# Optimization experiments

Measured on AMD Instinct MI355X. Metric: run time of the kernel, lower is better.

## Reference

```python
import jax, jax.numpy as jnp
import numpy as np

N_NODES = 32768
N_EDGES = 524288
N_FEAT = 256
HID = 256
N_GRAPHS = 64
N_CLASSES = 4
NODES_PER_GRAPH = N_NODES // N_GRAPHS
BN_EPS = 1e-5


def setup_inputs() -> dict:
    key = jax.random.key(0)
    ks = jax.random.split(key, 16)
    x = jax.random.normal(ks[0], (N_NODES, N_FEAT), dtype=jnp.float32)
    edge_index = jax.random.randint(ks[1], (2, N_EDGES), 0, N_NODES, dtype=jnp.int32)
    batch = (jnp.arange(N_NODES, dtype=jnp.int32) // NODES_PER_GRAPH)
    def xavier(k, shape):
        fan_in, fan_out = shape[0], shape[1]
        a = float(np.sqrt(6.0 / (fan_in + fan_out)))
        return jax.random.uniform(k, shape, jnp.float32, -a, a)
    return {
        "x": x, "edge_index": edge_index, "batch": batch,
        "W1": xavier(ks[2], (N_FEAT, HID)), "b1": jnp.zeros((HID,), jnp.float32),
        "g1": jnp.ones((HID,), jnp.float32), "be1": jnp.zeros((HID,), jnp.float32),
        "W2": xavier(ks[3], (HID, HID)), "b2": jnp.zeros((HID,), jnp.float32),
        "g2": jnp.ones((HID,), jnp.float32), "be2": jnp.zeros((HID,), jnp.float32),
        "W_ih": xavier(ks[4], (HID, 4 * HID)), "W_hh": xavier(ks[5], (HID, 4 * HID)),
        "b_ih": jnp.zeros((4 * HID,), jnp.float32), "b_hh": jnp.zeros((4 * HID,), jnp.float32),
        "W_fc": xavier(ks[6], (HID, N_CLASSES)), "b_fc": jnp.zeros((N_CLASSES,), jnp.float32),
    }


def gcn_conv(x, W, b, src, dst):
    # PyG GCNConv: add self-loops, symmetric normalization, aggregate, then bias
    h = x @ W                                   # [N, H]
    deg = jnp.zeros((x.shape[0],), h.dtype).at[dst].add(1.0) + 1.0  # in-deg + self-loop
    dinv = jax.lax.rsqrt(deg)
    coef = dinv[src] * dinv[dst]                # [E]
    msg = h[src] * coef[:, None]                # gather + scale, [E, H]
    agg = jnp.zeros_like(h).at[dst].add(msg)    # scatter-add
    agg = agg + h * (1.0 / deg)[:, None]        # self-loop term (norm = 1/deg)
    return agg + b


def batch_norm(x, gamma, beta):
    mean = jnp.mean(x, axis=0)
    var = jnp.mean(jnp.square(x - mean), axis=0)  # biased, as torch BN training
    return (x - mean) * jax.lax.rsqrt(var + BN_EPS) * gamma + beta


def reference(x, edge_index, batch, W1, b1, g1, be1, W2, b2, g2, be2,
              W_ih, W_hh, b_ih, b_hh, W_fc, b_fc):
    src, dst = edge_index[0], edge_index[1]
    h = jax.nn.relu(batch_norm(gcn_conv(x, W1, b1, src, dst), g1, be1))
    h = jax.nn.relu(batch_norm(gcn_conv(h, W2, b2, src, dst), g2, be2))
    # global mean pool over graphs
    sums = jax.ops.segment_sum(h, batch, num_segments=N_GRAPHS)
    cnts = jax.ops.segment_sum(jnp.ones((h.shape[0],), h.dtype), batch, num_segments=N_GRAPHS)
    pooled = sums / cnts[:, None]               # [G, H]
    # LSTM, seq_len = 1, zero initial state -> single cell step
    h0 = jnp.zeros((N_GRAPHS, HID), h.dtype)
    c0 = jnp.zeros((N_GRAPHS, HID), h.dtype)
    gates = pooled @ W_ih + h0 @ W_hh + b_ih + b_hh  # [G, 4H]
    i, f, g, o = jnp.split(gates, 4, axis=1)
    c1 = jax.nn.sigmoid(f) * c0 + jax.nn.sigmoid(i) * jnp.tanh(g)
    h1 = jax.nn.sigmoid(o) * jnp.tanh(c1)
    logits = h1 @ W_fc + b_fc
    logp = jax.nn.log_softmax(logits, axis=1)
    return (logp, (h1[None], c1[None]))
```

## Files before the change

kernel.cpp:

```cpp
#include <hip/hip_runtime.h>
#include <math.h>

#define N_NODES 32768
#define N_FEAT 256
#define HID 256
#define N_GRAPHS 64
#define NPG 512
#define N_CLASSES 4
#define BN_EPS 1e-5f

typedef __attribute__((ext_vector_type(8))) short bf16x8;
typedef __attribute__((ext_vector_type(4))) float f32x4;

__device__ __forceinline__ ushort f2b(float f) {
    union { float f; uint u; } v; v.f = f;
    uint u = v.u;
    return (ushort)((u + 0x7FFFu + ((u >> 16) & 1u)) >> 16);
}
__device__ __forceinline__ float bflo(uint u) {
    union { uint u; float f; } v; v.u = u << 16;
    return v.f;
}
__device__ __forceinline__ float bfhi(uint u) {
    union { uint u; float f; } v; v.u = u & 0xFFFF0000u;
    return v.f;
}

__global__ void k_count_prep(const int* __restrict__ dst, int* __restrict__ degcnt, int cntB,
                             const float* __restrict__ x, ushort* __restrict__ xb, int xB,
                             const float* __restrict__ W1, const float* __restrict__ W2,
                             ushort* __restrict__ Wt1, ushort* __restrict__ Wt2,
                             uint* __restrict__ csrs, int E) {
    int b = blockIdx.x;
    int t = threadIdx.x;
    if (b < cntB) {
        int e = b * 256 + t;
        if (e < E) atomicAdd(&degcnt[dst[e]], 1);
    } else if (b < cntB + xB) {
        int i = (b - cntB) * 256 + t;
        float4 v0 = *(const float4*)(x + (size_t)i * 8);
        float4 v1 = *(const float4*)(x + (size_t)i * 8 + 4);
        uint4 o;
        o.x = (uint)f2b(v0.x) | ((uint)f2b(v0.y) << 16);
        o.y = (uint)f2b(v0.z) | ((uint)f2b(v0.w) << 16);
        o.z = (uint)f2b(v1.x) | ((uint)f2b(v1.y) << 16);
        o.w = (uint)f2b(v1.z) | ((uint)f2b(v1.w) << 16);
        *(uint4*)(xb + (size_t)i * 8) = o;
    } else if (b < cntB + xB + 512) {
        int wb = b - cntB - xB;
        const float* W = (wb < 256) ? W1 : W2;
        ushort* Wt = (wb < 256) ? Wt1 : Wt2;
        int n = wb & 255;
        Wt[n * 256 + t] = f2b(W[t * 256 + n]);
    } else {
        int i = (b - cntB - xB - 512) * 256 + t;
        uint4 s = make_uint4(N_NODES, N_NODES, N_NODES, N_NODES);
        *(uint4*)(csrs + (size_t)i * 4) = s;
    }
}

__global__ __launch_bounds__(1024) void k_scan_all(const int* __restrict__ degcnt,
                                                   float* __restrict__ dinv,
                                                   int* __restrict__ row_start,
                                                   int* __restrict__ cursor,
                                                   uint* __restrict__ csrs,
                                                   ushort* __restrict__ hs_pad) {
    __shared__ int wsum[16];
    int t = threadIdx.x;
    int base = t * 32;
    int s = 0;
#pragma unroll
    for (int i = 0; i < 32; ++i) {
        int c = degcnt[base + i];
        s += (c + 2) & ~1;
    }
    int lane = t & 63, w = t >> 6;
    int v = s;
    for (int off = 1; off < 64; off <<= 1) {
        int u = __shfl_up(v, off);
        if (lane >= off) v += u;
    }
    if (lane == 63) wsum[w] = v;
    __syncthreads();
    if (t < 16) {
        int x = wsum[t];
        for (int off = 1; off < 16; off <<= 1) {
            int u = __shfl_up(x, off, 16);
            if (t >= off) x += u;
        }
        wsum[t] = x;
    }
    __syncthreads();
    int run = ((w > 0) ? wsum[w - 1] : 0) + v - s;
    for (int i = 0; i < 32; ++i) {
        int n = base + i;
        int c = degcnt[n];
        row_start[n] = run;
        csrs[run] = (uint)n;
        cursor[n] = run + 1;
        dinv[n] = rsqrtf((float)(c + 1));
        run += (c + 2) & ~1;
    }
    if (t == 0) row_start[N_NODES] = wsum[15];
    if (t < 128) ((uint*)hs_pad)[t] = 0;
}

__global__ void k_fill(const int* __restrict__ src, const int* __restrict__ dst,
                       int* __restrict__ cursor, uint* __restrict__ csrs, int E) {
    int e = blockIdx.x * 256 + threadIdx.x;
    if (e >= E) return;
    int d = dst[e];
    int pos = atomicAdd(&cursor[d], 1);
    csrs[pos] = (uint)src[e];
}

__global__ __launch_bounds__(256) void k_gemm_bf16(const ushort* __restrict__ A,
                                                   const ushort* __restrict__ Bt,
                                                   const float* __restrict__ dinv,
                                                   ushort* __restrict__ hs) {
    __shared__ ushort Bs[128 * 256];
    int tid = threadIdx.x;
    int n0 = blockIdx.x * 128;
    int m0 = blockIdx.y * 128;

#pragma unroll
    for (int c = 0; c < 16; ++c) {
        int g = c * 256 + tid;
        int idx = g * 8;
        int row = idx >> 8;
        int col = idx & 255;
        uint4 v = *(const uint4*)(Bt + (size_t)(n0 + row) * 256 + col);
        int sidx = idx ^ ((row & 7) << 3);
        *(uint4*)(Bs + sidx) = v;
    }
    __syncthreads();

    int wid = tid >> 6;
    int lane = tid & 63;
    int wr = wid >> 1, wc = wid & 1;
    int r = lane & 15;
    int ko = (lane >> 4) * 8;

    const ushort* Ab = A + (size_t)(m0 + wr * 64 + r) * 256 + ko;

    f32x4 acc[4][4] = {};
#pragma unroll
    for (int ks = 0; ks < 8; ++ks) {
        bf16x8 a[4], b[4];
#pragma unroll
        for (int i = 0; i < 4; ++i)
            a[i] = *(const bf16x8*)(Ab + i * (16 * 256) + ks * 32);
#pragma unroll
        for (int j = 0; j < 4; ++j) {
            int srow = wc * 64 + j * 16 + r;
            int idx = (srow * 256 + ko + ks * 32) ^ ((srow & 7) << 3);
            b[j] = *(const bf16x8*)(Bs + idx);
        }
#pragma unroll
        for (int i = 0; i < 4; ++i)
#pragma unroll
            for (int j = 0; j < 4; ++j)
                acc[i][j] = __builtin_amdgcn_mfma_f32_16x16x32_bf16(a[i], b[j], acc[i][j], 0, 0, 0);
    }

    int rr = (lane >> 4) * 4;
    int cc = lane & 15;
#pragma unroll
    for (int i = 0; i < 4; ++i) {
        int row = m0 + wr * 64 + i * 16 + rr;
#pragma unroll
        for (int r2 = 0; r2 < 4; ++r2) {
            float dv = dinv[row + r2];
#pragma unroll
            for (int j = 0; j < 4; ++j) {
                int col = n0 + wc * 64 + j * 16 + cc;
                hs[(size_t)(row + r2) * 256 + col] = f2b(acc[i][j][r2] * dv);
            }
        }
    }
}

__global__ __launch_bounds__(256) void k_agg(const ushort* __restrict__ hs,
                                             const uint* __restrict__ csrs,
                                             const int* __restrict__ row_start,
                                             const float* __restrict__ dinv,
                                             const float* __restrict__ bias,
                                             ushort* __restrict__ aggb) {
    int wid = threadIdx.x >> 6;
    int lane = threadIdx.x & 63;
    int half = lane >> 5;
    int fq = lane & 31;
    int n = blockIdx.x * 4 + wid;

    float dv = dinv[n];
    int base = row_start[n];
    int pairs = (row_start[n + 1] - base) >> 1;

    float a0 = 0.f, a1 = 0.f, a2 = 0.f, a3 = 0.f, a4 = 0.f, a5 = 0.f, a6 = 0.f, a7 = 0.f;

    int t = 0;
    for (; t + 4 <= pairs; t += 4) {
        uint s0 = csrs[base + 2 * t + 0 + half];
        uint s1 = csrs[base + 2 * t + 2 + half];
        uint s2 = csrs[base + 2 * t + 4 + half];
        uint s3 = csrs[base + 2 * t + 6 + half];
        uint4 h0 = *(const uint4*)(hs + (size_t)s0 * 256 + fq * 8);
        uint4 h1 = *(const uint4*)(hs + (size_t)s1 * 256 + fq * 8);
        uint4 h2 = *(const uint4*)(hs + (size_t)s2 * 256 + fq * 8);
        uint4 h3 = *(const uint4*)(hs + (size_t)s3 * 256 + fq * 8);
        a0 += bflo(h0.x) + bflo(h1.x) + bflo(h2.x) + bflo(h3.x);
        a1 += bfhi(h0.x) + bfhi(h1.x) + bfhi(h2.x) + bfhi(h3.x);
        a2 += bflo(h0.y) + bflo(h1.y) + bflo(h2.y) + bflo(h3.y);
        a3 += bfhi(h0.y) + bfhi(h1.y) + bfhi(h2.y) + bfhi(h3.y);
        a4 += bflo(h0.z) + bflo(h1.z) + bflo(h2.z) + bflo(h3.z);
        a5 += bfhi(h0.z) + bfhi(h1.z) + bfhi(h2.z) + bfhi(h3.z);
        a6 += bflo(h0.w) + bflo(h1.w) + bflo(h2.w) + bflo(h3.w);
        a7 += bfhi(h0.w) + bfhi(h1.w) + bfhi(h2.w) + bfhi(h3.w);
    }
    for (; t < pairs; ++t) {
        uint s0 = csrs[base + 2 * t + half];
        uint4 h0 = *(const uint4*)(hs + (size_t)s0 * 256 + fq * 8);
        a0 += bflo(h0.x); a1 += bfhi(h0.x);
        a2 += bflo(h0.y); a3 += bfhi(h0.y);
        a4 += bflo(h0.z); a5 += bfhi(h0.z);
        a6 += bflo(h0.w); a7 += bfhi(h0.w);
    }

    a0 += __shfl_xor(a0, 32); a1 += __shfl_xor(a1, 32);
    a2 += __shfl_xor(a2, 32); a3 += __shfl_xor(a3, 32);
    a4 += __shfl_xor(a4, 32); a5 += __shfl_xor(a5, 32);
    a6 += __shfl_xor(a6, 32); a7 += __shfl_xor(a7, 32);

    if (half == 0) {
        float4 b0 = *(const float4*)&bias[fq * 8];
        float4 b1 = *(const float4*)&bias[fq * 8 + 4];
        float o0 = a0 * dv + b0.x, o1 = a1 * dv + b0.y;
        float o2 = a2 * dv + b0.z, o3 = a3 * dv + b0.w;
        float o4 = a4 * dv + b1.x, o5 = a5 * dv + b1.y;
        float o6 = a6 * dv + b1.z, o7 = a7 * dv + b1.w;
        uint4 ov;
        ov.x = (uint)f2b(o0) | ((uint)f2b(o1) << 16);
        ov.y = (uint)f2b(o2) | ((uint)f2b(o3) << 16);
        ov.z = (uint)f2b(o4) | ((uint)f2b(o5) << 16);
        ov.w = (uint)f2b(o6) | ((uint)f2b(o7) << 16);
        *(uint4*)(aggb + (size_t)n * HID + fq * 8) = ov;
    }
}

__global__ __launch_bounds__(256) void k_bn_stats(const ushort* __restrict__ aggb,
                                                  float* __restrict__ bnsum,
                                                  float* __restrict__ bnsq) {
    int t = threadIdx.x;
    int fq = t & 31;
    int rg = t >> 5;
    int r0 = blockIdx.x * 128 + rg * 16;

    float s[8] = {}, q[8] = {};
    for (int r = 0; r < 16; ++r) {
        uint4 v = *(const uint4*)(aggb + (size_t)(r0 + r) * HID + fq * 8);
        float f0 = bflo(v.x), f1 = bfhi(v.x), f2 = bflo(v.y), f3 = bfhi(v.y);
        float f4 = bflo(v.z), f5 = bfhi(v.z), f6 = bflo(v.w), f7 = bfhi(v.w);
        s[0] += f0; q[0] += f0 * f0;  s[1] += f1; q[1] += f1 * f1;
        s[2] += f2; q[2] += f2 * f2;  s[3] += f3; q[3] += f3 * f3;
        s[4] += f4; q[4] += f4 * f4;  s[5] += f5; q[5] += f5 * f5;
        s[6] += f6; q[6] += f6 * f6;  s[7] += f7; q[7] += f7 * f7;
    }

    __shared__ float red[8][32][16];
#pragma unroll
    for (int i = 0; i < 8; ++i) {
        red[rg][fq][i] = s[i];
        red[rg][fq][8 + i] = q[i];
    }
    __syncthreads();
    int fq2 = t & 31;
    int vg = t >> 5;
#pragma unroll
    for (int k = 0; k < 2; ++k) {
        int v = vg * 2 + k;
        float acc = 0.f;
#pragma unroll
        for (int rgi = 0; rgi < 8; ++rgi) acc += red[rgi][fq2][v];
        float* dstp = (v < 8) ? bnsum : bnsq;
        atomicAdd(&dstp[fq2 * 8 + (v & 7)], acc);
    }
}

__global__ void k_bn_apply_b(const ushort* __restrict__ x, const float* __restrict__ bnsum,
                             const float* __restrict__ bnsq, const float* __restrict__ gamma,
                             const float* __restrict__ beta, ushort* __restrict__ out) {
    int i = blockIdx.x * 256 + threadIdx.x;
    if (i >= N_NODES * HID / 4) return;
    int f = (i & 63) * 4;
    const float invN = 1.0f / (float)N_NODES;
    uint2 v = *(const uint2*)(x + (size_t)i * 4);
    float vv[4] = {bflo(v.x), bfhi(v.x), bflo(v.y), bfhi(v.y)};
    float r[4];
#pragma unroll
    for (int qq = 0; qq < 4; ++qq) {
        float mean = bnsum[f + qq] * invN;
        float var = bnsq[f + qq] * invN - mean * mean;
        float t = (vv[qq] - mean) * rsqrtf(var + BN_EPS) * gamma[f + qq] + beta[f + qq];
        r[qq] = t > 0.0f ? t : 0.0f;
    }
    uint2 o;
    o.x = (uint)f2b(r[0]) | ((uint)f2b(r[1]) << 16);
    o.y = (uint)f2b(r[2]) | ((uint)f2b(r[3]) << 16);
    *(uint2*)(out + (size_t)i * 4) = o;
}

__global__ __launch_bounds__(256) void k_bn_pool(const ushort* __restrict__ aggb,
                                                 const float* __restrict__ bnsum,
                                                 const float* __restrict__ bnsq,
                                                 const float* __restrict__ gamma,
                                                 const float* __restrict__ beta,
                                                 float* __restrict__ pooled) {
    int g = blockIdx.x >> 4;
    int blk = blockIdx.x & 15;
    int f = threadIdx.x;
    const float invN = 1.0f / (float)N_NODES;
    float mean = bnsum[f] * invN;
    float var = bnsq[f] * invN - mean * mean;
    float sc = rsqrtf(var + BN_EPS) * gamma[f];
    float sh = beta[f] - mean * sc;
    int r0 = g * NPG + blk * 32;
    float s = 0.0f;
#pragma unroll 4
    for (int r = 0; r < 32; ++r) {
        float v = bflo((uint)aggb[(size_t)(r0 + r) * HID + f]) * sc + sh;
        s += v > 0.0f ? v : 0.0f;
    }
    atomicAdd(&pooled[g * HID + f], s);
}

__global__ __launch_bounds__(256) void k_head(const float* __restrict__ pooled,
                                              const float* __restrict__ W_ih,
                                              const float* __restrict__ b_ih,
                                              const float* __restrict__ b_hh,
                                              const float* __restrict__ W_fc,
                                              const float* __restrict__ b_fc,
                                              float* __restrict__ out) {
    __shared__ float p[HID];
    __shared__ float lsum[N_CLASSES][256];
    __shared__ float logits[N_CLASSES];
    int g = blockIdx.x, j = threadIdx.x;
    p[j] = pooled[g * HID + j] * (1.0f / (float)NPG);
    __syncthreads();

    float gi = 0.f, gf = 0.f, gg = 0.f, go = 0.f;
#pragma unroll 4
    for (int k = 0; k < HID; ++k) {
        float pk = p[k];
        const float* w = &W_ih[(size_t)k * (4 * HID) + j];
        gi += pk * w[0];
        gf += pk * w[HID];
        gg += pk * w[2 * HID];
        go += pk * w[3 * HID];
    }
    gi += b_ih[j] + b_hh[j];
    gf += b_ih[HID + j] + b_hh[HID + j];
    gg += b_ih[2 * HID + j] + b_hh[2 * HID + j];
    go += b_ih[3 * HID + j] + b_hh[3 * HID + j];
    (void)gf;

    float si = 1.f / (1.f + expf(-gi));
    float so = 1.f / (1.f + expf(-go));
    float c1 = si * tanhf(gg);
    float h1 = so * tanhf(c1);

    out[N_GRAPHS * N_CLASSES + g * HID + j] = h1;
    out[N_GRAPHS * N_CLASSES + N_GRAPHS * HID + g * HID + j] = c1;

#pragma unroll
    for (int c = 0; c < N_CLASSES; ++c)
        lsum[c][j] = h1 * W_fc[j * N_CLASSES + c];
    __syncthreads();
    for (int s = 128; s > 0; s >>= 1) {
        if (j < s) {
#pragma unroll
            for (int c = 0; c < N_CLASSES; ++c)
                lsum[c][j] += lsum[c][j + s];
        }
        __syncthreads();
    }
    if (j < N_CLASSES) logits[j] = lsum[j][0] + b_fc[j];
    __syncthreads();
    if (j < N_CLASSES) {
        float m = fmaxf(fmaxf(logits[0], logits[1]), fmaxf(logits[2], logits[3]));
        float lse = m + logf(expf(logits[0] - m) + expf(logits[1] - m) +
                             expf(logits[2] - m) + expf(logits[3] - m));
        out[g * N_CLASSES + j] = logits[j] - lse;
    }
}

extern "C" void kernel_launch(void* const* d_in, const int* in_sizes, int n_in,
                              void* d_out, int out_size, void* d_ws, size_t ws_size,
                              hipStream_t stream) {
    const float* x    = (const float*)d_in[0];
    const int*   ei   = (const int*)d_in[1];
    const float* W1   = (const float*)d_in[3];
    const float* b1   = (const float*)d_in[4];
    const float* g1   = (const float*)d_in[5];
    const float* be1  = (const float*)d_in[6];
    const float* W2   = (const float*)d_in[7];
    const float* b2   = (const float*)d_in[8];
    const float* g2   = (const float*)d_in[9];
    const float* be2  = (const float*)d_in[10];
    const float* W_ih = (const float*)d_in[11];
    const float* b_ih = (const float*)d_in[13];
    const float* b_hh = (const float*)d_in[14];
    const float* W_fc = (const float*)d_in[15];
    const float* b_fc = (const float*)d_in[16];
    float* out = (float*)d_out;

    int E = in_sizes[1] / 2;
    const int* src = ei;
    const int* dst = ei + E;

    const size_t MAT = (size_t)N_NODES * HID;
    size_t SZ = ((size_t)E + 2 * N_NODES + 1023) & ~(size_t)1023;

    ushort* aggb = (ushort*)d_ws;
    ushort* xb   = aggb + MAT;
    ushort* hs   = xb + MAT;
    ushort* Wt1  = hs + MAT + 256;
    ushort* Wt2  = Wt1 + 65536;
    float*  dinv = (float*)(Wt2 + 65536);
    int*    row_start = (int*)(dinv + N_NODES);
    int*    cursor    = row_start + N_NODES + 2;
    uint*   csrs      = (uint*)(cursor + N_NODES);
    int*    degcnt = (int*)(csrs + SZ);
    float*  bn1sum = (float*)(degcnt + N_NODES);
    float*  bn1sq  = bn1sum + HID;
    float*  bn2sum = bn1sq + HID;
    float*  bn2sq  = bn2sum + HID;
    float*  pooled = bn2sq + HID;
    size_t zeroBytes = (size_t)N_NODES * 4 + 4 * HID * 4 + (size_t)N_GRAPHS * HID * 4;

    dim3 blk(256);
    int edgeBlocks = (E + 255) / 256;
    int n8blk = (int)(MAT / 8 / 256);
    int sentB = (int)(SZ / 1024);
    int vec4Blocks = (int)(MAT / 4 / 256);
    int aggBlocks = N_NODES / 4;
    dim3 gemmGrid(2, N_NODES / 128);

    hipMemsetAsync(degcnt, 0, zeroBytes, stream);

    k_count_prep<<<edgeBlocks + n8blk + 512 + sentB, blk, 0, stream>>>(
        dst, degcnt, edgeBlocks, x, xb, n8blk, W1, W2, Wt1, Wt2, csrs, E);
    k_scan_all<<<1, dim3(1024), 0, stream>>>(degcnt, dinv, row_start, cursor, csrs,
                                             hs + MAT);
    k_fill<<<edgeBlocks, blk, 0, stream>>>(src, dst, cursor, csrs, E);

    k_gemm_bf16<<<gemmGrid, blk, 0, stream>>>(xb, Wt1, dinv, hs);
    k_agg<<<aggBlocks, blk, 0, stream>>>(hs, csrs, row_start, dinv, b1, aggb);
    k_bn_stats<<<N_NODES / 128, blk, 0, stream>>>(aggb, bn1sum, bn1sq);
    k_bn_apply_b<<<vec4Blocks, blk, 0, stream>>>(aggb, bn1sum, bn1sq, g1, be1, xb);

    k_gemm_bf16<<<gemmGrid, blk, 0, stream>>>(xb, Wt2, dinv, hs);
    k_agg<<<aggBlocks, blk, 0, stream>>>(hs, csrs, row_start, dinv, b2, aggb);
    k_bn_stats<<<N_NODES / 128, blk, 0, stream>>>(aggb, bn2sum, bn2sq);
    k_bn_pool<<<N_GRAPHS * 16, blk, 0, stream>>>(aggb, bn2sum, bn2sq, g2, be2, pooled);

    k_head<<<N_GRAPHS, blk, 0, stream>>>(pooled, W_ih, b_ih, b_hh, W_fc, b_fc, out);
}
```

Before: 324.1 us.

## Replace single-block degree scan with three-pass multi-block prefix scan

The single 1024-thread block that scanned all 32768 degree counts and wrote row_start, cursor, csrs sentinels and dinv is split into three kernels: per-block reduction, a 128-entry block-offset scan, and a parallel per-node scan-and-write across 128 blocks. The old kernel ran serial 32-element loops per thread on one CU, with strided writes that coalesce poorly. The new path spreads that work over many CUs at the cost of two extra kernel launches and a round trip through global memory for the block sums.

```diff
diff --git a/kernel.cpp b/kernel.cpp
--- a/kernel.cpp
+++ b/kernel.cpp
@@ -59,50 +59,69 @@
     }
 }
 
-__global__ __launch_bounds__(1024) void k_scan_all(const int* __restrict__ degcnt,
-                                                   float* __restrict__ dinv,
-                                                   int* __restrict__ row_start,
-                                                   int* __restrict__ cursor,
-                                                   uint* __restrict__ csrs,
-                                                   ushort* __restrict__ hs_pad) {
-    __shared__ int wsum[16];
+__global__ __launch_bounds__(256) void k_scan1(const int* __restrict__ degcnt,
+                                               int* __restrict__ blocksum) {
+    int n = blockIdx.x * 256 + threadIdx.x;
+    int p = (degcnt[n] + 2) & ~1;
+#pragma unroll
+    for (int off = 1; off < 64; off <<= 1) p += __shfl_xor(p, off);
+    __shared__ int ws[4];
+    int lane = threadIdx.x & 63, w = threadIdx.x >> 6;
+    if (lane == 0) ws[w] = p;
+    __syncthreads();
+    if (threadIdx.x == 0)
+        blocksum[blockIdx.x] = ws[0] + ws[1] + ws[2] + ws[3];
+}
+
+__global__ __launch_bounds__(128) void k_scan2(const int* __restrict__ blocksum,
+                                               int* __restrict__ blockoff,
+                                               int* __restrict__ row_start,
+                                               ushort* __restrict__ hs_pad) {
     int t = threadIdx.x;
-    int base = t * 32;
-    int s = 0;
-#pragma unroll
-    for (int i = 0; i < 32; ++i) {
-        int c = degcnt[base + i];
-        s += (c + 2) & ~1;
-    }
+    int v = blocksum[t];
     int lane = t & 63, w = t >> 6;
-    int v = s;
+    int inc = v;
+#pragma unroll
     for (int off = 1; off < 64; off <<= 1) {
-        int u = __shfl_up(v, off);
-        if (lane >= off) v += u;
-    }
-    if (lane == 63) wsum[w] = v;
-    __syncthreads();
-    if (t < 16) {
-        int x = wsum[t];
-        for (int off = 1; off < 16; off <<= 1) {
-            int u = __shfl_up(x, off, 16);
-            if (t >= off) x += u;
-        }
-        wsum[t] = x;
-    }
-    __syncthreads();
-    int run = ((w > 0) ? wsum[w - 1] : 0) + v - s;
-    for (int i = 0; i < 32; ++i) {
-        int n = base + i;
-        int c = degcnt[n];
-        row_start[n] = run;
-        csrs[run] = (uint)n;
-        cursor[n] = run + 1;
-        dinv[n] = rsqrtf((float)(c + 1));
-        run += (c + 2) & ~1;
-    }
-    if (t == 0) row_start[N_NODES] = wsum[15];
-    if (t < 128) ((uint*)hs_pad)[t] = 0;
+        int u = __shfl_up(inc, off);
+        if (lane >= off) inc += u;
+    }
+    __shared__ int w0tot;
+    if (t == 63) w0tot = inc;
+    __syncthreads();
+    if (w == 1) inc += w0tot;
+    blockoff[t] = inc - v;
+    if (t == 127) row_start[N_NODES] = inc;
+    ((uint*)hs_pad)[t] = 0;
+}
+
+__global__ __launch_bounds__(256) void k_scan3(const int* __restrict__ degcnt,
+                                               const int* __restrict__ blockoff,
+                                               float* __restrict__ dinv,
+                                               int* __restrict__ row_start,
+                                               int* __restrict__ cursor,
+                                               uint* __restrict__ csrs) {
+    int t = threadIdx.x;
+    int n = blockIdx.x * 256 + t;
+    int c = degcnt[n];
+    int p = (c + 2) & ~1;
+    int lane = t & 63, w = t >> 6;
+    int inc = p;
+#pragma unroll
+    for (int off = 1; off < 64; off <<= 1) {
+        int u = __shfl_up(inc, off);
+        if (lane >= off) inc += u;
+    }
+    __shared__ int ws[4];
+    if (lane == 63) ws[w] = inc;
+    __syncthreads();
+    int wadd = 0;
+    for (int i = 0; i < w; ++i) wadd += ws[i];
+    int run = blockoff[blockIdx.x] + wadd + inc - p;
+    row_start[n] = run;
+    csrs[run] = (uint)n;
+    cursor[n] = run + 1;
+    dinv[n] = rsqrtf((float)(c + 1));
 }
 
 __global__ void k_fill(const int* __restrict__ src, const int* __restrict__ dst,
@@ -429,7 +448,9 @@
     int*    row_start = (int*)(dinv + N_NODES);
     int*    cursor    = row_start + N_NODES + 2;
     uint*   csrs      = (uint*)(cursor + N_NODES);
-    int*    degcnt = (int*)(csrs + SZ);
+    int*    blocksum  = (int*)(csrs + SZ);
+    int*    blockoff  = blocksum + 128;
+    int*    degcnt = blockoff + 128;
     float*  bn1sum = (float*)(degcnt + N_NODES);
     float*  bn1sq  = bn1sum + HID;
     float*  bn2sum = bn1sq + HID;
@@ -449,8 +470,9 @@
 
     k_count_prep<<<edgeBlocks + n8blk + 512 + sentB, blk, 0, stream>>>(
         dst, degcnt, edgeBlocks, x, xb, n8blk, W1, W2, Wt1, Wt2, csrs, E);
-    k_scan_all<<<1, dim3(1024), 0, stream>>>(degcnt, dinv, row_start, cursor, csrs,
-                                             hs + MAT);
+    k_scan1<<<N_NODES / 256, blk, 0, stream>>>(degcnt, blocksum);
+    k_scan2<<<1, dim3(128), 0, stream>>>(blocksum, blockoff, row_start, hs + MAT);
+    k_scan3<<<N_NODES / 256, blk, 0, stream>>>(degcnt, blockoff, dinv, row_start, cursor, csrs);
     k_fill<<<edgeBlocks, blk, 0, stream>>>(src, dst, cursor, csrs, E);
 
     k_gemm_bf16<<<gemmGrid, blk, 0, stream>>>(xb, Wt1, dinv, hs);
```

New measurement: 286.6 us. 11.6% less time.
